# Kernel optimization log

Hardware: AMD Instinct MI355X
Metric: run time of the kernel (lower is better)

## Reference

```python
import jax, jax.numpy as jnp
import numpy as np

BS = 64          # BSR block size
B, D_IN, H, D_OUT = 4096, 1024, 4096, 1024
DENSITY = 0.5    # fraction of nonzero 64x64 blocks in fc2


def setup_inputs() -> dict:
    key = jax.random.key(0)
    ks = jax.random.split(key, 4)
    x = jax.random.normal(ks[0], (B, D_IN), jnp.float32)
    w1 = jax.random.normal(ks[1], (H, D_IN), jnp.float32) * (1.0 / np.sqrt(D_IN))
    b1 = jnp.zeros((H,), jnp.float32)
    w3 = jax.random.normal(ks[2], (D_OUT, H), jnp.float32) * (1.0 / np.sqrt(H))
    b3 = jnp.zeros((D_OUT,), jnp.float32)
    # Build BSR structure for fc2 weight [H, H]: block grid is (H//BS, H//BS)
    nbr, nbc = H // BS, H // BS
    rng = np.random.default_rng(0)
    mask = rng.random((nbr, nbc)) < DENSITY
    mask[:, 0] = True  # ensure each block row has at least one block
    crow = np.concatenate([[0], np.cumsum(mask.sum(axis=1))]).astype(np.int32)
    col = np.concatenate([np.nonzero(mask[r])[0] for r in range(nbr)]).astype(np.int32)
    nnzb = int(col.shape[0])
    values = jax.random.normal(ks[3], (nnzb, BS, BS), jnp.float32) * (1.0 / np.sqrt(H))
    return {
        "x": x, "w1": w1, "b1": b1,
        "values": values, "w3": w3, "b3": b3,
        "crow_indices": jnp.asarray(crow),
        "col_indices": jnp.asarray(col),
    }


def bsr_linear(x, crow, col, values, n_block_rows):
    """y = x @ W.T where W [out, in] is BSR with blocks values[nnzb, bs, bs]."""
    bsz = x.shape[0]
    bs = values.shape[1]
    nnzb = col.shape[0]
    # block row index of each nonzero block, from CSR row pointers
    block_row = jnp.searchsorted(crow, jnp.arange(nnzb, dtype=crow.dtype), side='right') - 1
    xb = x.reshape(bsz, -1, bs)            # [B, n_block_cols, bs]
    gath = xb[:, col]                      # [B, nnzb, bs] irregular gather
    # per-block contribution: block is W[row_blk, col_blk] of shape [bs_out, bs_in]
    contrib = jnp.einsum('bni,noi->nbo', gath, values)  # [nnzb, B, bs]
    yb = jax.ops.segment_sum(contrib, block_row, num_segments=n_block_rows)  # [nbr, B, bs]
    return yb.transpose(1, 0, 2).reshape(bsz, n_block_rows * bs)


def reference(x, w1, b1, values, w3, b3, crow_indices, col_indices):
    # Flatten is a no-op for 2D input
    h = jax.nn.relu(x @ w1.T + b1)                                   # fc1 + ReLU
    h = jax.nn.relu(bsr_linear(h, crow_indices, col_indices, values, H // BS))  # BSR fc2 + ReLU
    return h @ w3.T + b3                                             # fc3
```

## Files before the change

### kernel.cpp

```cpp
#include <hip/hip_runtime.h>
#include <hip/hip_bf16.h>
#include <stdint.h>


typedef __attribute__((ext_vector_type(4))) float f32x4;
typedef __attribute__((ext_vector_type(8))) __bf16 bf16x8;

#define DEV static __device__ __forceinline__

DEV ushort f2bf(float f) {
  union { float f; uint32_t u; } v; v.f = f;
  uint32_t r = v.u + 0x7fffu + ((v.u >> 16) & 1u);
  return (ushort)(r >> 16);
}

DEV void gld_lds16(const void* g, void* l) {
  __builtin_amdgcn_global_load_lds(
      (const __attribute__((address_space(1))) void*)g,
      (__attribute__((address_space(3))) void*)l, 16, 0, 0);
}

__global__ void cvt_kernel(const float* __restrict__ in, ushort* __restrict__ out, int n) {
  int i = (blockIdx.x * blockDim.x + threadIdx.x) * 4;
  if (i >= n) return;
  float4 v = *(const float4*)(in + i);
  ushort4 o;
  o.x = f2bf(v.x); o.y = f2bf(v.y); o.z = f2bf(v.z); o.w = f2bf(v.w);
  *(ushort4*)(out + i) = o;
}

template <bool RELU, bool OUT_BF16>
__global__ __launch_bounds__(256)
void gemm_nt(const ushort* __restrict__ A, const ushort* __restrict__ W,
             const float* __restrict__ bias, void* __restrict__ Cv,
             int K, int lda, int ldw, int ldc) {
  __shared__ ushort As[128 * 64];
  __shared__ ushort Ws[128 * 64];
  const int tid = threadIdx.x;
  const int wid = tid >> 6, lane = tid & 63;
  const int wm = wid >> 1, wn = wid & 1;
  const int i0 = blockIdx.y * 128, j0 = blockIdx.x * 128;
  f32x4 acc[4][4] = {};

  const int lrow = lane >> 3;
  const int lcol = (lane & 7) * 16;

  for (int k0 = 0; k0 < K; k0 += 64) {
#pragma unroll
    for (int i = 0; i < 4; ++i) {
      int ch = wid * 4 + i;
      int row = ch * 8 + lrow;
      const char* ga = (const char*)A + ((size_t)(i0 + row) * lda + k0) * 2 + lcol;
      gld_lds16(ga, (char*)As + ch * 1024);
      const char* gw = (const char*)W + ((size_t)(j0 + row) * ldw + k0) * 2 + lcol;
      gld_lds16(gw, (char*)Ws + ch * 1024);
    }
    __syncthreads();
#pragma unroll
    for (int kk = 0; kk < 64; kk += 32) {
      const int cl = lane & 15;
      const int kg = kk + (lane >> 4) * 8;
      bf16x8 a[4], b[4];
#pragma unroll
      for (int m = 0; m < 4; ++m)
        a[m] = *(const bf16x8*)&As[(wm * 64 + m * 16 + cl) * 64 + kg];
#pragma unroll
      for (int n = 0; n < 4; ++n)
        b[n] = *(const bf16x8*)&Ws[(wn * 64 + n * 16 + cl) * 64 + kg];
#pragma unroll
      for (int m = 0; m < 4; ++m)
#pragma unroll
        for (int n = 0; n < 4; ++n)
          acc[m][n] = __builtin_amdgcn_mfma_f32_16x16x32_bf16(a[m], b[n], acc[m][n], 0, 0, 0);
    }
    __syncthreads();
  }

  const int cl = lane & 15, r4 = (lane >> 4) * 4;
#pragma unroll
  for (int n = 0; n < 4; ++n) {
    int col = j0 + wn * 64 + n * 16 + cl;
    float bv = bias ? bias[col] : 0.0f;
#pragma unroll
    for (int m = 0; m < 4; ++m) {
      int rowb = i0 + wm * 64 + m * 16 + r4;
#pragma unroll
      for (int r = 0; r < 4; ++r) {
        float v = acc[m][n][r] + bv;
        if (RELU) v = fmaxf(v, 0.0f);
        if (OUT_BF16)
          ((ushort*)Cv)[(size_t)(rowb + r) * ldc + col] = f2bf(v);
        else
          ((float*)Cv)[(size_t)(rowb + r) * ldc + col] = v;
      }
    }
  }
}

__global__ __launch_bounds__(256)
void bsr_gemm(const ushort* __restrict__ A, const ushort* __restrict__ V,
              const int* __restrict__ crow, const int* __restrict__ colind,
              ushort* __restrict__ C, int Hdim) {
  __shared__ ushort As[2][256 * 64];
  __shared__ ushort Vs[2][64 * 64];
  const int tid = threadIdx.x;
  const int wid = tid >> 6, lane = tid & 63;

  const int bid = blockIdx.x;
  const int xcd = bid & 7;
  const int j = bid >> 3;
  const int tile = xcd + 8 * (j & 1);
  const int br = j >> 1;
  const int i0 = tile * 256;

  f32x4 acc[4][4] = {};
  const int n0 = crow[br], n1 = crow[br + 1];

  const int lr = lane >> 3;
  const int gsw = ((lane & 7) ^ lr) * 16;

  auto stage = [&](int buf, int n) {
    const int c = colind[n];
    const char* Abase = (const char*)A + ((size_t)i0 * Hdim + (size_t)c * 64) * 2;
#pragma unroll
    for (int i = 0; i < 8; ++i) {
      int ch = wid * 8 + i;
      int row = ch * 8 + lr;
      gld_lds16(Abase + (size_t)row * Hdim * 2 + gsw, (char*)As[buf] + ch * 1024);
    }
    const char* Vbase = (const char*)V + (size_t)n * 8192;
#pragma unroll
    for (int i = 0; i < 2; ++i) {
      int ch = wid * 2 + i;
      int row = ch * 8 + lr;
      gld_lds16(Vbase + row * 128 + gsw, (char*)Vs[buf] + ch * 1024);
    }
  };

  auto compute = [&](int buf) {
#pragma unroll
    for (int kk = 0; kk < 64; kk += 32) {
      const int cl = lane & 15;
      const int kg = kk + (lane >> 4) * 8;
      const int kx = kg ^ ((cl & 7) << 3);
      bf16x8 a[4], b[4];
#pragma unroll
      for (int m = 0; m < 4; ++m) {
        int row = wid * 64 + m * 16 + cl;
        a[m] = *(const bf16x8*)&As[buf][row * 64 + kx];
      }
#pragma unroll
      for (int nn = 0; nn < 4; ++nn) {
        int row = nn * 16 + cl;
        b[nn] = *(const bf16x8*)&Vs[buf][row * 64 + kx];
      }
      __builtin_amdgcn_s_setprio(1);
#pragma unroll
      for (int m = 0; m < 4; ++m)
#pragma unroll
        for (int nn = 0; nn < 4; ++nn)
          acc[m][nn] = __builtin_amdgcn_mfma_f32_16x16x32_bf16(a[m], b[nn], acc[m][nn], 0, 0, 0);
      __builtin_amdgcn_s_setprio(0);
    }
  };

  int cur = 0;
  stage(0, n0);
  __syncthreads();
  for (int n = n0; n < n1; ++n) {
    if (n + 1 < n1) stage(cur ^ 1, n + 1);
    compute(cur);
    __syncthreads();
    cur ^= 1;
  }

  const int cl = lane & 15, r4 = (lane >> 4) * 4;
#pragma unroll
  for (int nn = 0; nn < 4; ++nn) {
    int col = br * 64 + nn * 16 + cl;
#pragma unroll
    for (int m = 0; m < 4; ++m) {
      int rowb = i0 + wid * 64 + m * 16 + r4;
#pragma unroll
      for (int r = 0; r < 4; ++r) {
        float v = fmaxf(acc[m][nn][r], 0.0f);
        C[(size_t)(rowb + r) * Hdim + col] = f2bf(v);
      }
    }
  }
}

extern "C" void kernel_launch(void* const* d_in, const int* in_sizes, int n_in,
                              void* d_out, int out_size, void* d_ws, size_t ws_size,
                              hipStream_t stream) {
  const float* x    = (const float*)d_in[0];
  const float* w1   = (const float*)d_in[1];
  const float* b1   = (const float*)d_in[2];
  const float* vals = (const float*)d_in[3];
  const float* w3   = (const float*)d_in[4];
  const float* b3   = (const float*)d_in[5];
  const int* crow   = (const int*)d_in[6];
  const int* colind = (const int*)d_in[7];

  const int Bb = 4096, Din = 1024, H = 4096, Dout = 1024;
  const int nnzb = in_sizes[7];

  char* ws = (char*)d_ws;
  ushort* xb  = (ushort*)ws; ws += (size_t)Bb * Din * 2;
  ushort* w1b = (ushort*)ws; ws += (size_t)H * Din * 2;
  ushort* w3b = (ushort*)ws; ws += (size_t)Dout * H * 2;
  ushort* vb  = (ushort*)ws; ws += (size_t)nnzb * 64 * 64 * 2;
  ushort* h1b = (ushort*)ws; ws += (size_t)Bb * H * 2;
  ushort* h2b = (ushort*)ws; ws += (size_t)Bb * H * 2;

  auto cvt = [&](const float* src, ushort* dst, size_t n) {
    int blocks = (int)((n / 4 + 255) / 256);
    hipLaunchKernelGGL(cvt_kernel, dim3(blocks), dim3(256), 0, stream, src, dst, (int)n);
  };
  cvt(x, xb, (size_t)Bb * Din);
  cvt(w1, w1b, (size_t)H * Din);
  cvt(w3, w3b, (size_t)Dout * H);
  cvt(vals, vb, (size_t)nnzb * 4096);

  hipLaunchKernelGGL((gemm_nt<true, true>), dim3(H / 128, Bb / 128), dim3(256), 0, stream,
                     xb, w1b, b1, (void*)h1b, Din, Din, Din, H);
  hipLaunchKernelGGL(bsr_gemm, dim3((Bb / 256) * (H / 64)), dim3(256), 0, stream,
                     h1b, vb, crow, colind, h2b, H);
  hipLaunchKernelGGL((gemm_nt<false, false>), dim3(Dout / 128, Bb / 128), dim3(256), 0, stream,
                     h2b, w3b, b3, d_out, H, H, H, Dout);
}
```

Baseline: 252.7 us.

## Triple-buffer BSR GEMM with 8 waves and vmcnt-based prefetch waits

Moves the BSR block GEMM from a double buffer to a three-slot LDS ring, so two blocks are prefetched ahead and the wait for each block uses a fine-grained s_waitcnt vmcnt plus a raw barrier instead of __syncthreads. The workgroup doubles to 512 threads, each wave covering 32 rows instead of 64, which halves the accumulators per wave and adds more waves to hide latency. LDS use grows to about 120KB per block, which limits residency to one workgroup per CU. Correctness relies on the vmcnt count matching the five loads issued per stage.

Result: slower. 314.7 us (+24.5%).

```diff
diff --git a/kernel.cpp b/kernel.cpp
--- a/kernel.cpp
+++ b/kernel.cpp
@@ -97,12 +97,12 @@
   }
 }
 
-__global__ __launch_bounds__(256)
+__global__ __launch_bounds__(512)
 void bsr_gemm(const ushort* __restrict__ A, const ushort* __restrict__ V,
               const int* __restrict__ crow, const int* __restrict__ colind,
               ushort* __restrict__ C, int Hdim) {
-  __shared__ ushort As[2][256 * 64];
-  __shared__ ushort Vs[2][64 * 64];
+  __shared__ ushort As[3][256 * 64];
+  __shared__ ushort Vs[3][64 * 64];
   const int tid = threadIdx.x;
   const int wid = tid >> 6, lane = tid & 63;
 
@@ -113,50 +113,42 @@
   const int br = j >> 1;
   const int i0 = tile * 256;
 
-  f32x4 acc[4][4] = {};
+  f32x4 acc[2][4] = {};
   const int n0 = crow[br], n1 = crow[br + 1];
+  const int nt = n1 - n0;
 
   const int lr = lane >> 3;
   const int gsw = ((lane & 7) ^ lr) * 16;
 
-  auto stage = [&](int buf, int n) {
-    const int c = colind[n];
+  auto stage = [&](int slot, int n) {
+    const int c = colind[n0 + n];
     const char* Abase = (const char*)A + ((size_t)i0 * Hdim + (size_t)c * 64) * 2;
 #pragma unroll
-    for (int i = 0; i < 8; ++i) {
-      int ch = wid * 8 + i;
+    for (int i = 0; i < 4; ++i) {
+      int ch = wid * 4 + i;
       int row = ch * 8 + lr;
-      gld_lds16(Abase + (size_t)row * Hdim * 2 + gsw, (char*)As[buf] + ch * 1024);
-    }
-    const char* Vbase = (const char*)V + (size_t)n * 8192;
-#pragma unroll
-    for (int i = 0; i < 2; ++i) {
-      int ch = wid * 2 + i;
-      int row = ch * 8 + lr;
-      gld_lds16(Vbase + row * 128 + gsw, (char*)Vs[buf] + ch * 1024);
-    }
+      gld_lds16(Abase + (size_t)row * Hdim * 2 + gsw, (char*)As[slot] + ch * 1024);
+    }
+    const char* Vbase = (const char*)V + (size_t)(n0 + n) * 8192;
+    gld_lds16(Vbase + (wid * 8 + lr) * 128 + gsw, (char*)Vs[slot] + wid * 1024);
   };
 
-  auto compute = [&](int buf) {
+  auto compute = [&](int slot) {
 #pragma unroll
     for (int kk = 0; kk < 64; kk += 32) {
       const int cl = lane & 15;
       const int kg = kk + (lane >> 4) * 8;
       const int kx = kg ^ ((cl & 7) << 3);
-      bf16x8 a[4], b[4];
-#pragma unroll
-      for (int m = 0; m < 4; ++m) {
-        int row = wid * 64 + m * 16 + cl;
-        a[m] = *(const bf16x8*)&As[buf][row * 64 + kx];
-      }
-#pragma unroll
-      for (int nn = 0; nn < 4; ++nn) {
-        int row = nn * 16 + cl;
-        b[nn] = *(const bf16x8*)&Vs[buf][row * 64 + kx];
-      }
+      bf16x8 a[2], b[4];
+#pragma unroll
+      for (int m = 0; m < 2; ++m)
+        a[m] = *(const bf16x8*)&As[slot][(wid * 32 + m * 16 + cl) * 64 + kx];
+#pragma unroll
+      for (int nn = 0; nn < 4; ++nn)
+        b[nn] = *(const bf16x8*)&Vs[slot][(nn * 16 + cl) * 64 + kx];
       __builtin_amdgcn_s_setprio(1);
 #pragma unroll
-      for (int m = 0; m < 4; ++m)
+      for (int m = 0; m < 2; ++m)
 #pragma unroll
         for (int nn = 0; nn < 4; ++nn)
           acc[m][nn] = __builtin_amdgcn_mfma_f32_16x16x32_bf16(a[m], b[nn], acc[m][nn], 0, 0, 0);
@@ -164,14 +156,15 @@
     }
   };
 
-  int cur = 0;
-  stage(0, n0);
-  __syncthreads();
-  for (int n = n0; n < n1; ++n) {
-    if (n + 1 < n1) stage(cur ^ 1, n + 1);
-    compute(cur);
-    __syncthreads();
-    cur ^= 1;
+  if (nt > 0) stage(0, 0);
+  if (nt > 1) stage(1, 1);
+
+  for (int n = 0; n < nt; ++n) {
+    if (n + 1 < nt) asm volatile("s_waitcnt vmcnt(5)" ::: "memory");
+    else            asm volatile("s_waitcnt vmcnt(0)" ::: "memory");
+    asm volatile("s_barrier" ::: "memory");
+    if (n + 2 < nt) stage((n + 2) % 3, n + 2);
+    compute(n % 3);
   }
 
   const int cl = lane & 15, r4 = (lane >> 4) * 4;
@@ -179,8 +172,8 @@
   for (int nn = 0; nn < 4; ++nn) {
     int col = br * 64 + nn * 16 + cl;
 #pragma unroll
-    for (int m = 0; m < 4; ++m) {
-      int rowb = i0 + wid * 64 + m * 16 + r4;
+    for (int m = 0; m < 2; ++m) {
+      int rowb = i0 + wid * 32 + m * 16 + r4;
 #pragma unroll
       for (int r = 0; r < 4; ++r) {
         float v = fmaxf(acc[m][nn][r], 0.0f);
@@ -224,7 +217,7 @@
 
   hipLaunchKernelGGL((gemm_nt<true, true>), dim3(H / 128, Bb / 128), dim3(256), 0, stream,
                      xb, w1b, b1, (void*)h1b, Din, Din, Din, H);
-  hipLaunchKernelGGL(bsr_gemm, dim3((Bb / 256) * (H / 64)), dim3(256), 0, stream,
+  hipLaunchKernelGGL(bsr_gemm, dim3((Bb / 256) * (H / 64)), dim3(512), 0, stream,
                      h1b, vb, crow, colind, h2b, H);
   hipLaunchKernelGGL((gemm_nt<false, false>), dim3(Dout / 128, Bb / 128), dim3(256), 0, stream,
                      h2b, w3b, b3, d_out, H, H, H, Dout);
```

## Load BSR activation tiles directly into registers and triple-buffer weight blocks

Applied to the files above, without the earlier changes.

The BSR kernel no longer stages the 256x64 activation tile through LDS. Each wave now loads its own A fragments straight from global memory into double-buffered registers, while the 64x64 weight blocks go through a three-slot LDS ring. Column indices are cached in LDS, and synchronisation uses explicit vmcnt waits plus raw barriers instead of __syncthreads. This removes LDS traffic and capacity for A and should allow more occupancy and deeper prefetch. The cost is higher register pressure, uncoalesced 16-byte row loads, and reliance on hand-counted vmcnt values being exactly right.

Result: slower. 374.2 us (+48.1%).

```diff
diff --git a/kernel.cpp b/kernel.cpp
--- a/kernel.cpp
+++ b/kernel.cpp
@@ -101,8 +101,8 @@
 void bsr_gemm(const ushort* __restrict__ A, const ushort* __restrict__ V,
               const int* __restrict__ crow, const int* __restrict__ colind,
               ushort* __restrict__ C, int Hdim) {
-  __shared__ ushort As[2][256 * 64];
-  __shared__ ushort Vs[2][64 * 64];
+  __shared__ ushort Vs[3][64 * 64];
+  __shared__ int colLds[64];
   const int tid = threadIdx.x;
   const int wid = tid >> 6, lane = tid & 63;
 
@@ -113,68 +113,86 @@
   const int br = j >> 1;
   const int i0 = tile * 256;
 
-  f32x4 acc[4][4] = {};
-  const int n0 = crow[br], n1 = crow[br + 1];
+  const int n0 = crow[br];
+  const int nt = crow[br + 1] - n0;
+
+  if (tid < nt) colLds[tid] = colind[n0 + tid];
+  __syncthreads();
 
   const int lr = lane >> 3;
   const int gsw = ((lane & 7) ^ lr) * 16;
-
-  auto stage = [&](int buf, int n) {
-    const int c = colind[n];
-    const char* Abase = (const char*)A + ((size_t)i0 * Hdim + (size_t)c * 64) * 2;
-#pragma unroll
-    for (int i = 0; i < 8; ++i) {
-      int ch = wid * 8 + i;
-      int row = ch * 8 + lr;
-      gld_lds16(Abase + (size_t)row * Hdim * 2 + gsw, (char*)As[buf] + ch * 1024);
-    }
-    const char* Vbase = (const char*)V + (size_t)n * 8192;
+  const int cl = lane & 15;
+  const int kb = (lane >> 4) * 8;
+  const int kxor = (cl & 7) << 3;
+
+  f32x4 acc[4][4] = {};
+
+  const ushort* Abase = A + (size_t)(i0 + wid * 64 + cl) * Hdim + kb;
+
+  auto loadA = [&](bf16x8 (&dst)[4][2], int n) {
+    const int c = colLds[n];
+    const ushort* p = Abase + c * 64;
+#pragma unroll
+    for (int m = 0; m < 4; ++m)
+#pragma unroll
+      for (int kk = 0; kk < 2; ++kk)
+        dst[m][kk] = *(const bf16x8*)(p + (size_t)m * 16 * Hdim + kk * 32);
+  };
+  auto stageV = [&](int slot, int n) {
+    const char* Vb = (const char*)V + (size_t)(n0 + n) * 8192;
 #pragma unroll
     for (int i = 0; i < 2; ++i) {
       int ch = wid * 2 + i;
-      int row = ch * 8 + lr;
-      gld_lds16(Vbase + row * 128 + gsw, (char*)Vs[buf] + ch * 1024);
-    }
-  };
-
-  auto compute = [&](int buf) {
-#pragma unroll
-    for (int kk = 0; kk < 64; kk += 32) {
-      const int cl = lane & 15;
-      const int kg = kk + (lane >> 4) * 8;
-      const int kx = kg ^ ((cl & 7) << 3);
-      bf16x8 a[4], b[4];
-#pragma unroll
-      for (int m = 0; m < 4; ++m) {
-        int row = wid * 64 + m * 16 + cl;
-        a[m] = *(const bf16x8*)&As[buf][row * 64 + kx];
-      }
-#pragma unroll
-      for (int nn = 0; nn < 4; ++nn) {
-        int row = nn * 16 + cl;
-        b[nn] = *(const bf16x8*)&Vs[buf][row * 64 + kx];
-      }
+      gld_lds16(Vb + (ch * 8 + lr) * 128 + gsw, (char*)Vs[slot] + ch * 1024);
+    }
+  };
+
+  bf16x8 aP[4][2], aQ[4][2];
+
+  loadA(aP, 0);
+  stageV(0, 0);
+  if (nt > 1) {
+    stageV(1, 1);
+    asm volatile("s_waitcnt vmcnt(2)" ::: "memory");
+  } else {
+    asm volatile("s_waitcnt vmcnt(0)" ::: "memory");
+  }
+  __builtin_amdgcn_s_barrier();
+
+  auto body = [&](int n, bf16x8 (&cur)[4][2], bf16x8 (&nxt)[4][2]) {
+    const ushort* Vsl = Vs[n % 3];
+    if (n + 1 < nt) loadA(nxt, n + 1);
+    if (n + 2 < nt) stageV((n + 2) % 3, n + 2);
+#pragma unroll
+    for (int kk = 0; kk < 2; ++kk) {
+      const int kx = (kk * 32 + kb) ^ kxor;
+      bf16x8 b[4];
+#pragma unroll
+      for (int nn = 0; nn < 4; ++nn)
+        b[nn] = *(const bf16x8*)&Vsl[(nn * 16 + cl) * 64 + kx];
       __builtin_amdgcn_s_setprio(1);
 #pragma unroll
       for (int m = 0; m < 4; ++m)
 #pragma unroll
         for (int nn = 0; nn < 4; ++nn)
-          acc[m][nn] = __builtin_amdgcn_mfma_f32_16x16x32_bf16(a[m], b[nn], acc[m][nn], 0, 0, 0);
+          acc[m][nn] = __builtin_amdgcn_mfma_f32_16x16x32_bf16(cur[m][kk], b[nn], acc[m][nn], 0, 0, 0);
       __builtin_amdgcn_s_setprio(0);
     }
-  };
-
-  int cur = 0;
-  stage(0, n0);
-  __syncthreads();
-  for (int n = n0; n < n1; ++n) {
-    if (n + 1 < n1) stage(cur ^ 1, n + 1);
-    compute(cur);
-    __syncthreads();
-    cur ^= 1;
-  }
-
-  const int cl = lane & 15, r4 = (lane >> 4) * 4;
+    if (n + 1 < nt) {
+      if (n + 2 < nt) asm volatile("s_waitcnt vmcnt(10)" ::: "memory");
+      else            asm volatile("s_waitcnt vmcnt(8)" ::: "memory");
+      __builtin_amdgcn_s_barrier();
+    }
+  };
+
+  int n = 0;
+  while (n < nt) {
+    body(n, aP, aQ); ++n;
+    if (n >= nt) break;
+    body(n, aQ, aP); ++n;
+  }
+
+  const int r4 = (lane >> 4) * 4;
 #pragma unroll
   for (int nn = 0; nn < 4; ++nn) {
     int col = br * 64 + nn * 16 + cl;
```
